# Kernel tuning notes

Hardware: AMD Instinct MI355X
Metric: run time of the kernel (lower is better)

## Reference

```python
import jax, jax.numpy as jnp
import numpy as np

NUM_MODELS = 64
LAYERS = 5
OUTPUT_EVERY = 2


def _mr_linear(x, idx, W, b):
    # Faithful to MultiResnetLinear: gather a full (B, out, in) weight tensor
    # per sample via indices, then batched matvec + gathered bias.
    return jnp.einsum('boi,bi->bo', W[idx], x) + b[idx]


def setup_inputs() -> dict:
    key = jax.random.key(0)
    ks = jax.random.split(key, 11)
    B, F_IN, HID, F_OUT = 65536, 6, 64, 3
    sk = float(np.sqrt(1.0 / NUM_MODELS))

    def u(k, shape):
        # 2*sqrt_k*rand - sqrt_k  ==  uniform(-sqrt_k, sqrt_k)
        return jax.random.uniform(k, shape, jnp.float32, -sk, sk)

    return {
        'inputs': jax.random.normal(ks[0], (B, F_IN), jnp.float32),
        'W0': u(ks[1], (NUM_MODELS, HID, F_IN)), 'b0': u(ks[2], (NUM_MODELS, HID)),
        'W1': u(ks[3], (NUM_MODELS, HID, HID)), 'b1': u(ks[4], (NUM_MODELS, HID)),
        'W2': u(ks[5], (NUM_MODELS, HID, HID)), 'b2': u(ks[6], (NUM_MODELS, HID)),
        'W3': u(ks[7], (NUM_MODELS, HID, HID)), 'b3': u(ks[8], (NUM_MODELS, HID)),
        'Wf': u(ks[9], (NUM_MODELS, F_OUT, HID)), 'bf': u(ks[10], (NUM_MODELS, F_OUT)),
    }


def reference(inputs, W0, b0, W1, b1, W2, b2, W3, b3, Wf, bf):
    B = inputs.shape[0]
    two_pi = 2.0 * np.pi
    # 'angle' selection mode: bucket ray azimuth into num_models bins
    angles = jnp.arctan2(inputs[:, 2], inputs[:, 0])
    angles = jnp.fmod(angles + two_pi, two_pi) / two_pi * NUM_MODELS
    selection_indices = jnp.floor(angles).astype(jnp.int32)
    selection_logits = jnp.ones((B, NUM_MODELS), inputs.dtype)
    selection_probabilities = jax.nn.softmax(selection_logits, axis=1)

    hidden_layers = [(W0, b0), (W1, b1), (W2, b2), (W3, b3)]
    model_outputs = []
    x = inputs
    for i in range(LAYERS - 1):
        x = jax.nn.relu(_mr_linear(x, selection_indices, *hidden_layers[i]))
        if (i + 1) % OUTPUT_EVERY == 0 and i != LAYERS - 2:
            model_outputs.append(_mr_linear(x, selection_indices, Wf, bf))
    model_outputs.append(_mr_linear(x, selection_indices, Wf, bf))
    model_outputs = jnp.stack(model_outputs, axis=1)  # (B, 2, 3)
    return model_outputs, selection_indices, selection_logits, selection_probabilities
```

## Files before the change

### kernel.cpp

```cpp
#include <hip/hip_runtime.h>
#include <math.h>

#define BTOT 65536
#define NM   64
#define FIN  6
#define HID  64
#define FOUT 3

#define MO_OFF  0
#define IDX_OFF 393216
#define LOG_OFF 458752
#define PRB_OFF 4653056
#define OUT_END 8847360

#define LCAP  2048

typedef __attribute__((ext_vector_type(8))) short short8v;
typedef __attribute__((ext_vector_type(4))) float f32x4;

union AB { uint u[4]; uint4 q; short8v v; };

static __device__ __forceinline__ uint pack_hi2(float a, float b) {
    return (__float_as_uint(b) & 0xFFFF0000u) | (__float_as_uint(a) >> 16);
}
static __device__ __forceinline__ float hi_part(float a) {
    return __uint_as_float(__float_as_uint(a) & 0xFFFF0000u);
}
static __device__ __forceinline__ void split8(const float (&e)[8], AB& hi, AB& lo) {
#pragma unroll
    for (int t = 0; t < 4; ++t) {
        float a = e[2 * t], b = e[2 * t + 1];
        hi.u[t] = pack_hi2(a, b);
        lo.u[t] = pack_hi2(a - hi_part(a), b - hi_part(b));
    }
}
static __device__ __forceinline__ uint bf16rn(float x) {
    uint u = __float_as_uint(x);
    return (u + 0x7FFFu + ((u >> 16) & 1u)) >> 16;
}
static __device__ __forceinline__ void round8(const float (&e)[8], AB& w) {
#pragma unroll
    for (int t = 0; t < 4; ++t)
        w.u[t] = (bf16rn(e[2 * t + 1]) << 16) | bf16rn(e[2 * t]);
}
static __device__ __forceinline__ f32x4 mf(const AB& a, const AB& b, f32x4 c) {
    return __builtin_amdgcn_mfma_f32_16x16x32_bf16(a.v, b.v, c, 0, 0, 0);
}
static __device__ __forceinline__ int permo(int t, int i) {
    return 32 * (i & 1) + 8 * (i >> 2) + 2 * t + ((i >> 1) & 1);
}

__global__ void k_index_fill(const float* __restrict__ in, float* __restrict__ out,
                             int* __restrict__ sorted2, int* __restrict__ cnt)
{
    __shared__ int lh[NM];
    const int tid = (int)threadIdx.x;
    const int bid = (int)blockIdx.x;

    if (tid < NM) lh[tid] = 0;
    __syncthreads();

    const int b = bid * 256 + tid;
    const float xv = in[b * 6 + 0];
    const float zv = in[b * 6 + 2];
    const float TWO_PI = 6.28318530717958647692f;
    float af = (float)atan2((double)zv, (double)xv);
    float t = fmodf(af + TWO_PI, TWO_PI) / TWO_PI * 64.0f;
    int idx = (int)floorf(t);
    idx = min(max(idx, 0), 63);

    out[IDX_OFF + b] = (float)idx;

    const int lrank = atomicAdd(&lh[idx], 1);
    sorted2[(idx * 256 + bid) * 256 + lrank] = b;
    __syncthreads();
    if (tid < NM) cnt[tid * 256 + bid] = lh[tid];

    float4* __restrict__ out4 = (float4*)out;
    const int start = LOG_OFF / 4;
    const int split = PRB_OFF / 4;
    const float4 ones = make_float4(1.0f, 1.0f, 1.0f, 1.0f);
    const float4 prob = make_float4(0.015625f, 0.015625f, 0.015625f, 0.015625f);
#pragma unroll
    for (int k = 0; k < 32; ++k) {
        const int i = start + k * 65536 + bid * 256 + tid;
        out4[i] = (i < split) ? ones : prob;
    }
}

#define NSETS 30
#define L1S   4
#define L2S   12
#define L3S   20
#define LFS   28

__global__ __launch_bounds__(512, 2) void k_mlp(
    const float* __restrict__ in,
    const float* __restrict__ W0, const float* __restrict__ B0,
    const float* __restrict__ W1, const float* __restrict__ B1,
    const float* __restrict__ W2, const float* __restrict__ B2,
    const float* __restrict__ W3, const float* __restrict__ B3,
    const float* __restrict__ WF, const float* __restrict__ BF,
    const int* __restrict__ sorted2, const int* __restrict__ cnt,
    float* __restrict__ out)
{
    __shared__ uint bhS[NSETS][64][4];
    __shared__ int list[LCAP];
    __shared__ int wtot[8];
    __shared__ int wbase[8];

    const int m = blockIdx.x;
    const int yy = (int)blockIdx.y;
    const int tid = (int)threadIdx.x;
    const int wid = tid >> 6;
    const int lane = tid & 63;
    const int g = lane >> 4;
    const int c16 = lane & 15;

    for (int job = tid; job < 3 * 512; job += 512) {
        const int ly = job >> 9;
        const int o  = (job >> 3) & 63;
        const int kc = job & 7;
        const float* Wl = (ly == 0) ? W1 : (ly == 1) ? W2 : W3;
        const float4* p = (const float4*)(Wl + m * (HID * HID) + o * HID + kc * 8);
        float4 f0 = p[0], f1 = p[1];
        float e[8] = {f0.x, f0.y, f0.z, f0.w, f1.x, f1.y, f1.z, f1.w};
        const int t  = (o >> 1) & 3;
        const int cq = ((o >> 5) & 1) | ((o & 1) << 1) | (((o >> 3) & 3) << 2);
        const int ks = kc >> 2, gq = kc & 3;
        AB w;
        round8(e, w);
        *(uint4*)&bhS[L1S + ly * 8 + ks * 4 + t][gq * 16 + cq][0] = w.q;
    }

    for (int job = tid; job < 6 * 64; job += 512) {
        const int s = job >> 6, ln = job & 63;
        const int set = (s < 4) ? s : (s + 24);
        const int gq = ln >> 4, cq = ln & 15;
        float e[8];
        if (set < 4) {
            const int o = permo(set, cq);
            if (gq == 0) {
                const float* w = W0 + m * (HID * FIN) + o * FIN;
#pragma unroll
                for (int j = 0; j < 8; ++j)
                    e[j] = (j < FIN) ? w[j] : ((j == 6) ? B0[m * HID + o] : 0.0f);
            } else {
#pragma unroll
                for (int j = 0; j < 8; ++j) e[j] = 0.0f;
            }
        } else {
            const int ks = set - 28;
            if (cq < FOUT) {
                const float* w = WF + m * (FOUT * HID) + cq * HID + ks * 32 + gq * 8;
#pragma unroll
                for (int j = 0; j < 8; ++j) e[j] = w[j];
            } else {
#pragma unroll
                for (int j = 0; j < 8; ++j) e[j] = 0.0f;
            }
        }
        AB w;
        round8(e, w);
        *(uint4*)&bhS[set][ln][0] = w.q;
    }

    const int cval = (tid < 256) ? cnt[m * 256 + tid] : 0;
    int isc = cval;
#pragma unroll
    for (int d = 1; d < 64; d <<= 1) {
        int y = __shfl_up(isc, d);
        if (lane >= d) isc += y;
    }
    if (lane == 63) wtot[wid] = isc;
    __syncthreads();
    {
        int run = 0;
#pragma unroll
        for (int w = 0; w < 8; ++w) { if (w == wid) wbase[wid] = run; run += wtot[w]; }
    }
    __syncthreads();
    const int n0 = wtot[0] + wtot[1] + wtot[2] + wtot[3];
    const int n = min(n0, LCAP);
    if (tid < 256 && cval > 0) {
        const int pos0 = wbase[wid] + (isc - cval);
        const uint4* src = (const uint4*)(sorted2 + (m * 256 + tid) * 256);
        for (int j = 0; j < cval; j += 4) {
            uint4 v4 = src[j >> 2];
#pragma unroll
            for (int k = 0; k < 4; ++k) {
                const int p = pos0 + j + k;
                if (j + k < cval && p < LCAP)
                    list[p] = (int)(((const uint*)&v4)[k]);
            }
        }
    }
    __syncthreads();

    AB lf[2];
#pragma unroll
    for (int ks = 0; ks < 2; ++ks)
        lf[ks].q = *(const uint4*)&bhS[LFS + ks][lane][0];
    const float bf0 = BF[m * FOUT + 0];
    const float bf1 = BF[m * FOUT + 1];
    const float bf2 = BF[m * FOUT + 2];

    const int nt = (n + 15) >> 4;
    for (int ti = yy * 8 + wid; ti < nt; ti += 64) {
        const int s = ti * 16 + c16;
        const bool act = (s < n);
        const int b = list[act ? s : (n - 1)];

        AB xh, xl;
        if (g == 0) {
            const float* xp = in + b * 6;
            float e[8] = {xp[0], xp[1], xp[2], xp[3], xp[4], xp[5], 1.0f, 0.0f};
            split8(e, xh, xl);
        } else {
#pragma unroll
            for (int t = 0; t < 4; ++t) { xh.u[t] = 0u; xl.u[t] = 0u; }
        }
        f32x4 acc[4];
#pragma unroll
        for (int t = 0; t < 4; ++t) {
            AB ah;
            ah.q = *(const uint4*)&bhS[t][lane][0];
            f32x4 cc = {0.0f, 0.0f, 0.0f, 0.0f};
            cc = mf(ah, xh, cc); cc = mf(ah, xl, cc);
            acc[t] = cc;
        }

        AB bh[2], bl[2];
#pragma unroll
        for (int ks = 0; ks < 2; ++ks) {
            float e[8];
#pragma unroll
            for (int jj = 0; jj < 8; ++jj)
                e[jj] = fmaxf(acc[jj >> 1][2 * (jj & 1) + ks], 0.0f);
            split8(e, bh[ks], bl[ks]);
        }

#define LAYERX(SET0)                                                          \
        _Pragma("unroll")                                                     \
        for (int ks = 0; ks < 2; ++ks)                                        \
        _Pragma("unroll")                                                     \
        for (int t = 0; t < 4; ++t) {                                         \
            AB ah;                                                            \
            ah.q = *(const uint4*)&bhS[(SET0) + ks * 4 + t][lane][0];          \
            f32x4 cc = (ks == 0) ? f32x4{0.0f, 0.0f, 0.0f, 0.0f} : acc[t];    \
            cc = mf(ah, bh[ks], cc);                                          \
            cc = mf(ah, bl[ks], cc);                                          \
            acc[t] = cc;                                                      \
        }

#define BUILDF(BPTR)                                                          \
        _Pragma("unroll")                                                     \
        for (int ks = 0; ks < 2; ++ks) {                                      \
            const float4* bp = (const float4*)((BPTR) + ks * 32 + g * 8);     \
            float4 q0 = bp[0], q1 = bp[1];                                    \
            float bb[8] = {q0.x, q0.y, q0.z, q0.w, q1.x, q1.y, q1.z, q1.w};   \
            float e[8];                                                       \
            _Pragma("unroll")                                                 \
            for (int jj = 0; jj < 8; ++jj)                                    \
                e[jj] = fmaxf(acc[jj >> 1][2 * (jj & 1) + ks] + bb[jj], 0.0f);\
            split8(e, bh[ks], bl[ks]);                                        \
        }

#define LFINX(PASS)                                                           \
        {                                                                     \
            f32x4 o = {bf0, bf1, bf2, 0.0f};                                  \
            _Pragma("unroll")                                                 \
            for (int ks = 0; ks < 2; ++ks) {                                  \
                o = mf(lf[ks], bh[ks], o);                                    \
                o = mf(lf[ks], bl[ks], o);                                    \
            }                                                                 \
            if (g == 0 && act) {                                              \
                float* p = out + MO_OFF + b * 6 + (PASS) * 3;                 \
                p[0] = o[0]; p[1] = o[1]; p[2] = o[2];                        \
            }                                                                 \
        }

        LAYERX(L1S);
        BUILDF(B1 + m * HID);
        LFINX(0);
        LAYERX(L2S);
        BUILDF(B2 + m * HID);
        LAYERX(L3S);
        BUILDF(B3 + m * HID);
        LFINX(1);
    }
}

extern "C" void kernel_launch(void* const* d_in, const int* in_sizes, int n_in,
                              void* d_out, int out_size, void* d_ws, size_t ws_size,
                              hipStream_t stream)
{
    const float* in = (const float*)d_in[0];
    const float* W0 = (const float*)d_in[1];
    const float* B0 = (const float*)d_in[2];
    const float* W1 = (const float*)d_in[3];
    const float* B1 = (const float*)d_in[4];
    const float* W2 = (const float*)d_in[5];
    const float* B2 = (const float*)d_in[6];
    const float* W3 = (const float*)d_in[7];
    const float* B3 = (const float*)d_in[8];
    const float* WF = (const float*)d_in[9];
    const float* BF = (const float*)d_in[10];
    float* out = (float*)d_out;

    int* sorted2 = (int*)d_ws;
    int* cnt     = sorted2 + NM * 256 * 256;

    k_index_fill<<<256, 256, 0, stream>>>(in, out, sorted2, cnt);
    k_mlp<<<dim3(NM, 8), 512, 0, stream>>>(in, W0, B0, W1, B1, W2, B2, W3, B3,
                                           WF, BF, sorted2, cnt, out);
}
```

Baseline: 32.37 us.

## Precompute bf16 weight fragments once per model and move constant fills into MLP

Weight conversion to bf16 MFMA fragment layout moves out of each of the 8 k_mlp blocks per model and into 64 extra blocks of the first kernel, which write it to workspace. k_mlp then just copies the prepared fragments into shared memory. The constant logits/probabilities fill moves from the index kernel into k_mlp, so those stores can overlap MLP work. The trade-off is an extra workspace round trip for the weights and more store traffic at the start of k_mlp.

```diff
diff --git a/kernel.cpp b/kernel.cpp
--- a/kernel.cpp
+++ b/kernel.cpp
@@ -50,57 +50,102 @@
     return 32 * (i & 1) + 8 * (i >> 2) + 2 * t + ((i >> 1) & 1);
 }
 
-__global__ void k_index_fill(const float* __restrict__ in, float* __restrict__ out,
-                             int* __restrict__ sorted2, int* __restrict__ cnt)
-{
-    __shared__ int lh[NM];
-    const int tid = (int)threadIdx.x;
-    const int bid = (int)blockIdx.x;
-
-    if (tid < NM) lh[tid] = 0;
-    __syncthreads();
-
-    const int b = bid * 256 + tid;
-    const float xv = in[b * 6 + 0];
-    const float zv = in[b * 6 + 2];
-    const float TWO_PI = 6.28318530717958647692f;
-    float af = (float)atan2((double)zv, (double)xv);
-    float t = fmodf(af + TWO_PI, TWO_PI) / TWO_PI * 64.0f;
-    int idx = (int)floorf(t);
-    idx = min(max(idx, 0), 63);
-
-    out[IDX_OFF + b] = (float)idx;
-
-    const int lrank = atomicAdd(&lh[idx], 1);
-    sorted2[(idx * 256 + bid) * 256 + lrank] = b;
-    __syncthreads();
-    if (tid < NM) cnt[tid * 256 + bid] = lh[tid];
-
-    float4* __restrict__ out4 = (float4*)out;
-    const int start = LOG_OFF / 4;
-    const int split = PRB_OFF / 4;
-    const float4 ones = make_float4(1.0f, 1.0f, 1.0f, 1.0f);
-    const float4 prob = make_float4(0.015625f, 0.015625f, 0.015625f, 0.015625f);
-#pragma unroll
-    for (int k = 0; k < 32; ++k) {
-        const int i = start + k * 65536 + bid * 256 + tid;
-        out4[i] = (i < split) ? ones : prob;
-    }
-}
-
 #define NSETS 30
 #define L1S   4
 #define L2S   12
 #define L3S   20
 #define LFS   28
 
+__global__ void k_index_conv(const float* __restrict__ in, float* __restrict__ out,
+                             int* __restrict__ sorted2, int* __restrict__ cnt,
+                             uint4* __restrict__ wsW4,
+                             const float* __restrict__ W0, const float* __restrict__ B0,
+                             const float* __restrict__ W1, const float* __restrict__ W2,
+                             const float* __restrict__ W3, const float* __restrict__ WF)
+{
+    __shared__ int lh[NM];
+    const int tid = (int)threadIdx.x;
+    const int bid = (int)blockIdx.x;
+
+    if (bid < 256) {
+        if (tid < NM) lh[tid] = 0;
+        __syncthreads();
+
+        const int b = bid * 256 + tid;
+        const float xv = in[b * 6 + 0];
+        const float zv = in[b * 6 + 2];
+        const float TWO_PI = 6.28318530717958647692f;
+        float af = (float)atan2((double)zv, (double)xv);
+        float t = fmodf(af + TWO_PI, TWO_PI) / TWO_PI * 64.0f;
+        int idx = (int)floorf(t);
+        idx = min(max(idx, 0), 63);
+
+        out[IDX_OFF + b] = (float)idx;
+
+        const int lrank = atomicAdd(&lh[idx], 1);
+        sorted2[(idx * 256 + bid) * 256 + lrank] = b;
+        __syncthreads();
+        if (tid < NM) cnt[tid * 256 + bid] = lh[tid];
+        return;
+    }
+
+    const int mm = bid - 256;
+    uint4* __restrict__ dst = wsW4 + mm * (NSETS * 64);
+
+    for (int job = tid; job < 3 * 512; job += 256) {
+        const int ly = job >> 9;
+        const int o  = (job >> 3) & 63;
+        const int kc = job & 7;
+        const float* Wl = (ly == 0) ? W1 : (ly == 1) ? W2 : W3;
+        const float4* p = (const float4*)(Wl + mm * (HID * HID) + o * HID + kc * 8);
+        float4 f0 = p[0], f1 = p[1];
+        float e[8] = {f0.x, f0.y, f0.z, f0.w, f1.x, f1.y, f1.z, f1.w};
+        const int t  = (o >> 1) & 3;
+        const int cq = ((o >> 5) & 1) | ((o & 1) << 1) | (((o >> 3) & 3) << 2);
+        const int ks = kc >> 2, gq = kc & 3;
+        AB w;
+        round8(e, w);
+        dst[(L1S + ly * 8 + ks * 4 + t) * 64 + gq * 16 + cq] = w.q;
+    }
+
+    for (int job = tid; job < 6 * 64; job += 256) {
+        const int s = job >> 6, ln = job & 63;
+        const int set = (s < 4) ? s : (s + 24);
+        const int gq = ln >> 4, cq = ln & 15;
+        float e[8];
+        if (set < 4) {
+            const int o = permo(set, cq);
+            if (gq == 0) {
+                const float* w = W0 + mm * (HID * FIN) + o * FIN;
+#pragma unroll
+                for (int j = 0; j < 8; ++j)
+                    e[j] = (j < FIN) ? w[j] : ((j == 6) ? B0[mm * HID + o] : 0.0f);
+            } else {
+#pragma unroll
+                for (int j = 0; j < 8; ++j) e[j] = 0.0f;
+            }
+        } else {
+            const int ks = set - 28;
+            if (cq < FOUT) {
+                const float* w = WF + mm * (FOUT * HID) + cq * HID + ks * 32 + gq * 8;
+#pragma unroll
+                for (int j = 0; j < 8; ++j) e[j] = w[j];
+            } else {
+#pragma unroll
+                for (int j = 0; j < 8; ++j) e[j] = 0.0f;
+            }
+        }
+        AB w;
+        round8(e, w);
+        dst[set * 64 + ln] = w.q;
+    }
+}
+
 __global__ __launch_bounds__(512, 2) void k_mlp(
     const float* __restrict__ in,
-    const float* __restrict__ W0, const float* __restrict__ B0,
-    const float* __restrict__ W1, const float* __restrict__ B1,
-    const float* __restrict__ W2, const float* __restrict__ B2,
-    const float* __restrict__ W3, const float* __restrict__ B3,
-    const float* __restrict__ WF, const float* __restrict__ BF,
+    const float* __restrict__ B1, const float* __restrict__ B2,
+    const float* __restrict__ B3, const float* __restrict__ BF,
+    const uint4* __restrict__ wsW4,
     const int* __restrict__ sorted2, const int* __restrict__ cnt,
     float* __restrict__ out)
 {
@@ -117,52 +162,12 @@
     const int g = lane >> 4;
     const int c16 = lane & 15;
 
-    for (int job = tid; job < 3 * 512; job += 512) {
-        const int ly = job >> 9;
-        const int o  = (job >> 3) & 63;
-        const int kc = job & 7;
-        const float* Wl = (ly == 0) ? W1 : (ly == 1) ? W2 : W3;
-        const float4* p = (const float4*)(Wl + m * (HID * HID) + o * HID + kc * 8);
-        float4 f0 = p[0], f1 = p[1];
-        float e[8] = {f0.x, f0.y, f0.z, f0.w, f1.x, f1.y, f1.z, f1.w};
-        const int t  = (o >> 1) & 3;
-        const int cq = ((o >> 5) & 1) | ((o & 1) << 1) | (((o >> 3) & 3) << 2);
-        const int ks = kc >> 2, gq = kc & 3;
-        AB w;
-        round8(e, w);
-        *(uint4*)&bhS[L1S + ly * 8 + ks * 4 + t][gq * 16 + cq][0] = w.q;
-    }
-
-    for (int job = tid; job < 6 * 64; job += 512) {
-        const int s = job >> 6, ln = job & 63;
-        const int set = (s < 4) ? s : (s + 24);
-        const int gq = ln >> 4, cq = ln & 15;
-        float e[8];
-        if (set < 4) {
-            const int o = permo(set, cq);
-            if (gq == 0) {
-                const float* w = W0 + m * (HID * FIN) + o * FIN;
-#pragma unroll
-                for (int j = 0; j < 8; ++j)
-                    e[j] = (j < FIN) ? w[j] : ((j == 6) ? B0[m * HID + o] : 0.0f);
-            } else {
-#pragma unroll
-                for (int j = 0; j < 8; ++j) e[j] = 0.0f;
-            }
-        } else {
-            const int ks = set - 28;
-            if (cq < FOUT) {
-                const float* w = WF + m * (FOUT * HID) + cq * HID + ks * 32 + gq * 8;
-#pragma unroll
-                for (int j = 0; j < 8; ++j) e[j] = w[j];
-            } else {
-#pragma unroll
-                for (int j = 0; j < 8; ++j) e[j] = 0.0f;
-            }
-        }
-        AB w;
-        round8(e, w);
-        *(uint4*)&bhS[set][ln][0] = w.q;
+    {
+        const uint4* src = wsW4 + m * (NSETS * 64);
+        for (int job = tid; job < NSETS * 64; job += 512) {
+            uint4 w = src[job];
+            *(uint4*)&bhS[job >> 6][job & 63][0] = w;
+        }
     }
 
     const int cval = (tid < 256) ? cnt[m * 256 + tid] : 0;
@@ -196,6 +201,19 @@
         }
     }
     __syncthreads();
+
+    {
+        float4* __restrict__ out4 = (float4*)out;
+        const int split = PRB_OFF / 4;
+        const float4 ones = make_float4(1.0f, 1.0f, 1.0f, 1.0f);
+        const float4 prob = make_float4(0.015625f, 0.015625f, 0.015625f, 0.015625f);
+        const int i0 = LOG_OFF / 4 + (yy * NM + m) * 4096 + tid;
+#pragma unroll
+        for (int k = 0; k < 8; ++k) {
+            const int i = i0 + k * 512;
+            out4[i] = (i < split) ? ones : prob;
+        }
+    }
 
     AB lf[2];
 #pragma unroll
@@ -308,10 +326,12 @@
     const float* BF = (const float*)d_in[10];
     float* out = (float*)d_out;
 
-    int* sorted2 = (int*)d_ws;
-    int* cnt     = sorted2 + NM * 256 * 256;
-
-    k_index_fill<<<256, 256, 0, stream>>>(in, out, sorted2, cnt);
-    k_mlp<<<dim3(NM, 8), 512, 0, stream>>>(in, W0, B0, W1, B1, W2, B2, W3, B3,
-                                           WF, BF, sorted2, cnt, out);
-}
+    int*  sorted2 = (int*)d_ws;
+    int*  cnt     = sorted2 + NM * 256 * 256;
+    uint4* wsW4   = (uint4*)(cnt + NM * 256);
+
+    k_index_conv<<<320, 256, 0, stream>>>(in, out, sorted2, cnt, wsW4,
+                                          W0, B0, W1, W2, W3, WF);
+    k_mlp<<<dim3(NM, 8), 512, 0, stream>>>(in, B1, B2, B3, BF, wsW4,
+                                           sorted2, cnt, out);
+}
```

Measured after the change: 31.86 us. No clear change (-1.6%).
